# Performance work log

Hardware: AMD Instinct MI355X
Metric: run time of the kernel (lower is better)

## Reference

```python
import jax, jax.numpy as jnp
import numpy as np

N = 100000   # nodes
E = 1600000  # edges (avg degree 16)
DIN = 128
DH = 64


def setup_inputs() -> dict:
    key = jax.random.key(0)
    ks = jax.random.split(key, 6)
    x = jax.random.normal(ks[0], (N, DIN), dtype=jnp.float32)
    edge_index = jax.random.randint(ks[1], (2, E), 0, N, dtype=jnp.int32)
    W1 = jax.random.normal(ks[2], (DIN, DH), dtype=jnp.float32) * (1.0 / np.sqrt(DIN))
    b1 = jnp.zeros((DH,), dtype=jnp.float32)
    W2 = jax.random.normal(ks[3], (DH, DH), dtype=jnp.float32) * (1.0 / np.sqrt(DH))
    b2 = jnp.zeros((DH,), dtype=jnp.float32)
    alpha = jnp.full((DH,), 0.25, dtype=jnp.float32)  # PReLU per-channel slope (torch default 0.25)
    return {"x": x, "edge_index": edge_index, "W1": W1, "b1": b1, "W2": W2, "b2": b2, "alpha": alpha}


def _gcn_layer(h, src, dst, norm, W, b):
    # GCNConv: linear transform, then normalized scatter-add aggregation, then bias
    h = h @ W                                  # [N, dout]
    msg = h[src] * norm[:, None]               # [E+N, dout] gathered + scaled messages
    agg = jax.ops.segment_sum(msg, dst, num_segments=N)
    return agg + b


def reference(x, edge_index, W1, b1, W2, b2, alpha):
    src0, dst0 = edge_index[0], edge_index[1]
    # GCNConv default: add self-loops, symmetric normalization deg^{-1/2} A deg^{-1/2}
    loops = jnp.arange(N, dtype=src0.dtype)
    src = jnp.concatenate([src0, loops])
    dst = jnp.concatenate([dst0, loops])
    ones = jnp.ones(src.shape[0], dtype=x.dtype)
    deg = jax.ops.segment_sum(ones, dst, num_segments=N)
    dinv = jnp.where(deg > 0, jax.lax.rsqrt(deg), 0.0)
    norm = dinv[src] * dinv[dst]               # [E+N]

    prelu = lambda z: jnp.where(z >= 0, z, alpha * z)  # shared per-channel PReLU
    z = prelu(_gcn_layer(x, src, dst, norm, W1, b1))
    z = prelu(_gcn_layer(z, src, dst, norm, W2, b2))
    return z
```

## Files before the change

kernel.cpp:

```cpp
#include <hip/hip_runtime.h>
#include <hip/hip_bf16.h>

#define NN 100000
#define NE 1600000
#define NBUCK 391
#define CAP 5056
#define CHUNK 2048
#define PBLOCKS 782
#define MMBLOCKS 782
#define BCUR_STRIDE 16

typedef __attribute__((ext_vector_type(8))) short short8;
typedef __attribute__((ext_vector_type(4))) float f32x4;

static __device__ __forceinline__ unsigned short f2bf(float f) {
    unsigned u = __float_as_uint(f);
    unsigned r = (u + 0x7fffu + ((u >> 16) & 1u)) >> 16;
    return (unsigned short)r;
}
static __device__ __forceinline__ float bf_lo(unsigned u) {
    return __uint_as_float(u << 16);
}
static __device__ __forceinline__ float bf_hi(unsigned u) {
    return __uint_as_float(u & 0xffff0000u);
}
static __device__ __forceinline__ void acc8(float* acc, uint4 v, float nm) {
    acc[0] += bf_lo(v.x) * nm; acc[1] += bf_hi(v.x) * nm;
    acc[2] += bf_lo(v.y) * nm; acc[3] += bf_hi(v.y) * nm;
    acc[4] += bf_lo(v.z) * nm; acc[5] += bf_hi(v.z) * nm;
    acc[6] += bf_lo(v.w) * nm; acc[7] += bf_hi(v.w) * nm;
}
static __device__ __forceinline__ void acc8a(float* acc, uint4 v) {
    acc[0] += bf_lo(v.x); acc[1] += bf_hi(v.x);
    acc[2] += bf_lo(v.y); acc[3] += bf_hi(v.y);
    acc[4] += bf_lo(v.z); acc[5] += bf_hi(v.z);
    acc[6] += bf_lo(v.w); acc[7] += bf_hi(v.w);
}

template<bool SCALED>
static __device__ __forceinline__ void agg_loop(const unsigned char* hb,
                                                const int* __restrict__ esrc,
                                                const float* __restrict__ dinv,
                                                int start, int cnt, float dn,
                                                float* acc) {
    int i = 0;
    for (; i + 4 <= cnt; i += 4) {
        int s0 = esrc[start + i];
        int s1 = esrc[start + i + 1];
        int s2 = esrc[start + i + 2];
        int s3 = esrc[start + i + 3];
        uint4 w0 = *(const uint4*)(hb + ((unsigned)s0 << 7));
        uint4 w1 = *(const uint4*)(hb + ((unsigned)s1 << 7));
        uint4 w2 = *(const uint4*)(hb + ((unsigned)s2 << 7));
        uint4 w3 = *(const uint4*)(hb + ((unsigned)s3 << 7));
        if constexpr (SCALED) {
            acc8a(acc, w0); acc8a(acc, w1); acc8a(acc, w2); acc8a(acc, w3);
        } else {
            float n0 = dinv[s0] * dn, n1 = dinv[s1] * dn;
            float n2 = dinv[s2] * dn, n3 = dinv[s3] * dn;
            acc8(acc, w0, n0); acc8(acc, w1, n1); acc8(acc, w2, n2); acc8(acc, w3, n3);
        }
    }
    for (; i < cnt; ++i) {
        int s0 = esrc[start + i];
        uint4 w0 = *(const uint4*)(hb + ((unsigned)s0 << 7));
        if constexpr (SCALED) {
            acc8a(acc, w0);
        } else {
            float n0 = dinv[s0] * dn;
            acc8(acc, w0, n0);
        }
    }
}

__global__ __launch_bounds__(256) void k_fat(const int* __restrict__ ei,
                                             int* __restrict__ bcur,
                                             unsigned* __restrict__ ebuf,
                                             const float* __restrict__ x,
                                             const float* __restrict__ W1,
                                             unsigned short* __restrict__ hout) {
    __shared__ __attribute__((aligned(16))) unsigned char smem[19584];
    int tid = threadIdx.x;
    if (blockIdx.x < PBLOCKS) {
        int* lexc  = (int*)smem;
        int* lbase = (int*)(smem + 1564);
        unsigned* sv = (unsigned*)(smem + 3128);
        int* sd    = (int*)(smem + 11320);
        int* wscan = (int*)(smem + 19512);
        int* sTot  = (int*)(smem + 19528);

        int e0 = blockIdx.x * CHUNK;
        for (int i = tid; i < NBUCK; i += 256) lexc[i] = 0;
        __syncthreads();
        int bs[8]; int rs[8]; unsigned ps[8];
        #pragma unroll
        for (int k = 0; k < 8; ++k) {
            int e = e0 + k * 256 + tid;
            bs[k] = -1;
            if (e < NE) {
                int d = ei[NE + e];
                int s = ei[e];
                int b = d >> 8;
                bs[k] = b;
                rs[k] = atomicAdd(&lexc[b], 1);
                ps[k] = ((unsigned)s << 8) | (unsigned)(d & 255);
            }
        }
        __syncthreads();
        int b0i = 2 * tid, b1i = 2 * tid + 1;
        int c0 = (b0i < NBUCK) ? lexc[b0i] : 0;
        int c1 = (b1i < NBUCK) ? lexc[b1i] : 0;
        int v = c0 + c1;
        int lane = tid & 63;
        int incl = v;
        #pragma unroll
        for (int off = 1; off < 64; off <<= 1) {
            int t = __shfl_up(incl, off, 64);
            if (lane >= off) incl += t;
        }
        if (lane == 63) wscan[tid >> 6] = incl;
        int gb0 = 0, gb1 = 0;
        if (c0) gb0 = atomicAdd(&bcur[b0i * BCUR_STRIDE], c0);
        if (c1) gb1 = atomicAdd(&bcur[b1i * BCUR_STRIDE], c1);
        __syncthreads();
        if (tid == 0) {
            int a = 0;
            #pragma unroll
            for (int w = 0; w < 4; ++w) { int t = wscan[w]; wscan[w] = a; a += t; }
            *sTot = a;
        }
        __syncthreads();
        int ex = incl - v + wscan[tid >> 6];
        if (b0i < NBUCK) { lexc[b0i] = ex;      lbase[b0i] = gb0; }
        if (b1i < NBUCK) { lexc[b1i] = ex + c0; lbase[b1i] = gb1; }
        __syncthreads();
        #pragma unroll
        for (int k = 0; k < 8; ++k) {
            if (bs[k] >= 0) {
                int b = bs[k];
                int slot = lexc[b] + rs[k];
                int pos  = lbase[b] + rs[k];
                sv[slot] = ps[k];
                sd[slot] = (pos < CAP) ? b * CAP + pos : -1;
            }
        }
        __syncthreads();
        int V = *sTot;
        for (int j = tid; j < V; j += 256) {
            int d = sd[j];
            if (d >= 0) ebuf[d] = sv[j];
        }
    } else {
        constexpr int K = 128, KP = K + 8;
        unsigned short* Wt = (unsigned short*)smem;
        for (int idx = tid; idx < K * 64; idx += 256) {
            int k = idx >> 6, n = idx & 63;
            Wt[n * KP + k] = f2bf(W1[idx]);
        }
        __syncthreads();
        int wave = tid >> 6, lane = tid & 63;
        int m = lane & 15, q = lane >> 4;
        int nb = (blockIdx.x - PBLOCKS) * 128 + wave * 32;
        #pragma unroll
        for (int rt = 0; rt < 2; ++rt) {
            int n0 = nb + rt * 16;
            f32x4 acc[4] = {{0.f,0.f,0.f,0.f},{0.f,0.f,0.f,0.f},{0.f,0.f,0.f,0.f},{0.f,0.f,0.f,0.f}};
            int row = n0 + m;
            int rowc = row < NN ? row : NN - 1;
            const float* xr = x + (long)rowc * K;
            #pragma unroll
            for (int kk = 0; kk < K / 32; ++kk) {
                const float4* p = (const float4*)(xr + kk * 32 + q * 8);
                float4 v0 = p[0], v1 = p[1];
                float xv[8] = {v0.x, v0.y, v0.z, v0.w, v1.x, v1.y, v1.z, v1.w};
                short8 afrag;
                #pragma unroll
                for (int i2 = 0; i2 < 8; ++i2) afrag[i2] = (short)f2bf(xv[i2]);
                #pragma unroll
                for (int nt = 0; nt < 4; ++nt) {
                    const short8* bp = (const short8*)&Wt[(nt * 16 + m) * KP + kk * 32 + q * 8];
                    acc[nt] = __builtin_amdgcn_mfma_f32_16x16x32_bf16(afrag, *bp, acc[nt], 0, 0, 0);
                }
            }
            #pragma unroll
            for (int reg = 0; reg < 4; ++reg) {
                int node = n0 + q * 4 + reg;
                if (node < NN) {
                    #pragma unroll
                    for (int nt = 0; nt < 4; ++nt)
                        hout[(long)node * 64 + nt * 16 + m] = f2bf(acc[nt][reg]);
                }
            }
        }
    }
}

__global__ __launch_bounds__(256) void k_build(const int* __restrict__ bcur,
                                               const unsigned* __restrict__ ebuf,
                                               unsigned* __restrict__ rowinfo,
                                               float* __restrict__ dinv,
                                               int* __restrict__ esrc) {
    __shared__ int cnt[2048];
    __shared__ int kstart[2048];
    __shared__ int wsum[4];
    int tid = threadIdx.x;
    int base = blockIdx.x * CAP;
    int nedge = bcur[blockIdx.x * BCUR_STRIDE];
    if (nedge > CAP) nedge = CAP;
    #pragma unroll
    for (int t = 0; t < 8; ++t) cnt[(tid << 3) | t] = 0;
    __syncthreads();
    int st[20];
    int ssrc[20];
    #pragma unroll
    for (int k = 0; k < 20; ++k) {
        int j = tid + k * 256;
        st[k] = -1;
        if (j < nedge) {
            unsigned p = ebuf[base + j];
            int dl = (int)(p & 255u);
            int s = (int)(p >> 8);
            int key = (dl << 3) | (s >> 14);
            int r = atomicAdd(&cnt[key], 1);
            st[k] = (r << 11) | key;
            ssrc[k] = s;
        }
    }
    __syncthreads();
    int c[8];
    int v = 0;
    #pragma unroll
    for (int t = 0; t < 8; ++t) { c[t] = cnt[(tid << 3) | t]; v += c[t]; }
    int lane = tid & 63;
    int incl = v;
    #pragma unroll
    for (int off = 1; off < 64; off <<= 1) {
        int t = __shfl_up(incl, off, 64);
        if (lane >= off) incl += t;
    }
    if (lane == 63) wsum[tid >> 6] = incl;
    __syncthreads();
    if (tid == 0) {
        int a = 0;
        #pragma unroll
        for (int w = 0; w < 4; ++w) { int t = wsum[w]; wsum[w] = a; a += t; }
    }
    __syncthreads();
    int ex = incl - v + wsum[tid >> 6];
    int node = blockIdx.x * 256 + tid;
    if (node < NN) {
        rowinfo[node] = ((unsigned)(base + ex) << 11) | (unsigned)v;
        dinv[node] = rsqrtf((float)(v + 1));
    }
    int off = base + ex;
    #pragma unroll
    for (int t = 0; t < 8; ++t) { kstart[(tid << 3) | t] = off; off += c[t]; }
    __syncthreads();
    #pragma unroll
    for (int k = 0; k < 20; ++k) {
        if (st[k] >= 0)
            esrc[kstart[st[k] & 2047] + (st[k] >> 11)] = ssrc[k];
    }
}

__global__ __launch_bounds__(256) void k_aggmm(const unsigned* __restrict__ rowinfo,
                                               const int* __restrict__ esrc,
                                               const unsigned short* __restrict__ h,
                                               const float* __restrict__ dinv,
                                               const float* __restrict__ bias,
                                               const float* __restrict__ alpha,
                                               const float* __restrict__ W2,
                                               unsigned short* __restrict__ hout2) {
    __shared__ unsigned short Wt[64 * 72];
    __shared__ unsigned short aggs[32 * 72];
    __shared__ float dnv[32];
    int tid = threadIdx.x;
    for (int idx = tid; idx < 64 * 64; idx += 256) {
        int k = idx >> 6, n = idx & 63;
        Wt[n * 72 + k] = f2bf(W2[idx]);
    }
    int sl = tid & 7;
    int ln = tid >> 3;
    int node = blockIdx.x * 32 + ln;
    unsigned u = rowinfo[node];
    int start = (int)(u >> 11);
    int cnt = (int)(u & 2047u);
    float dn = dinv[node];
    if (sl == 0) dnv[ln] = dn;
    const unsigned char* hb = (const unsigned char*)h + sl * 16;

    float acc[8];
    {
        uint4 hw = *(const uint4*)(hb + ((unsigned)node << 7));
        float d2 = dn * dn;
        acc[0] = bf_lo(hw.x) * d2; acc[1] = bf_hi(hw.x) * d2;
        acc[2] = bf_lo(hw.y) * d2; acc[3] = bf_hi(hw.y) * d2;
        acc[4] = bf_lo(hw.z) * d2; acc[5] = bf_hi(hw.z) * d2;
        acc[6] = bf_lo(hw.w) * d2; acc[7] = bf_hi(hw.w) * d2;
    }
    agg_loop<false>(hb, esrc, dinv, start, cnt, dn, acc);

    float4 blo = *(const float4*)(bias + sl * 8);
    float4 bhi = *(const float4*)(bias + sl * 8 + 4);
    float4 alo = *(const float4*)(alpha + sl * 8);
    float4 ahi = *(const float4*)(alpha + sl * 8 + 4);
    float bb[8] = {blo.x, blo.y, blo.z, blo.w, bhi.x, bhi.y, bhi.z, bhi.w};
    float aa[8] = {alo.x, alo.y, alo.z, alo.w, ahi.x, ahi.y, ahi.z, ahi.w};
    #pragma unroll
    for (int j = 0; j < 8; ++j) {
        float v = acc[j] + bb[j];
        acc[j] = v >= 0.f ? v : aa[j] * v;
    }
    uint4 pk;
    pk.x = (unsigned)f2bf(acc[0]) | ((unsigned)f2bf(acc[1]) << 16);
    pk.y = (unsigned)f2bf(acc[2]) | ((unsigned)f2bf(acc[3]) << 16);
    pk.z = (unsigned)f2bf(acc[4]) | ((unsigned)f2bf(acc[5]) << 16);
    pk.w = (unsigned)f2bf(acc[6]) | ((unsigned)f2bf(acc[7]) << 16);
    *(uint4*)&aggs[ln * 72 + sl * 8] = pk;
    __syncthreads();

    int wave = tid >> 6;
    if (wave < 2) {
        int lane = tid & 63;
        int m = lane & 15, q = lane >> 4;
        int row = wave * 16 + m;
        f32x4 c2[4] = {{0.f,0.f,0.f,0.f},{0.f,0.f,0.f,0.f},{0.f,0.f,0.f,0.f},{0.f,0.f,0.f,0.f}};
        #pragma unroll
        for (int kk = 0; kk < 2; ++kk) {
            short8 afrag = *(const short8*)&aggs[row * 72 + kk * 32 + q * 8];
            #pragma unroll
            for (int nt = 0; nt < 4; ++nt) {
                const short8* bp = (const short8*)&Wt[(nt * 16 + m) * 72 + kk * 32 + q * 8];
                c2[nt] = __builtin_amdgcn_mfma_f32_16x16x32_bf16(afrag, *bp, c2[nt], 0, 0, 0);
            }
        }
        #pragma unroll
        for (int reg = 0; reg < 4; ++reg) {
            int nd = blockIdx.x * 32 + wave * 16 + q * 4 + reg;
            float dv = dnv[wave * 16 + q * 4 + reg];
            #pragma unroll
            for (int nt = 0; nt < 4; ++nt)
                hout2[(long)nd * 64 + nt * 16 + m] = f2bf(c2[nt][reg] * dv);
        }
    }
}

__global__ __launch_bounds__(256) void k_agg2(const unsigned* __restrict__ rowinfo,
                                              const int* __restrict__ esrc,
                                              const unsigned short* __restrict__ h,
                                              const float* __restrict__ dinv,
                                              const float* __restrict__ bias,
                                              const float* __restrict__ alpha,
                                              float* __restrict__ out) {
    int sl = threadIdx.x & 7;
    int node = blockIdx.x * 32 + (threadIdx.x >> 3);
    unsigned u = rowinfo[node];
    int start = (int)(u >> 11);
    int cnt = (int)(u & 2047u);
    float dn = dinv[node];
    const unsigned char* hb = (const unsigned char*)h + sl * 16;

    float acc[8];
    {
        uint4 hw = *(const uint4*)(hb + ((unsigned)node << 7));
        acc[0] = bf_lo(hw.x); acc[1] = bf_hi(hw.x);
        acc[2] = bf_lo(hw.y); acc[3] = bf_hi(hw.y);
        acc[4] = bf_lo(hw.z); acc[5] = bf_hi(hw.z);
        acc[6] = bf_lo(hw.w); acc[7] = bf_hi(hw.w);
    }
    agg_loop<true>(hb, esrc, dinv, start, cnt, dn, acc);

    float4 blo = *(const float4*)(bias + sl * 8);
    float4 bhi = *(const float4*)(bias + sl * 8 + 4);
    float4 alo = *(const float4*)(alpha + sl * 8);
    float4 ahi = *(const float4*)(alpha + sl * 8 + 4);
    float bb[8] = {blo.x, blo.y, blo.z, blo.w, bhi.x, bhi.y, bhi.z, bhi.w};
    float aa[8] = {alo.x, alo.y, alo.z, alo.w, ahi.x, ahi.y, ahi.z, ahi.w};
    #pragma unroll
    for (int j = 0; j < 8; ++j) {
        float v = acc[j] * dn + bb[j];
        acc[j] = v >= 0.f ? v : aa[j] * v;
    }
    float* op = out + (long)node * 64 + sl * 8;
    *(float4*)op = make_float4(acc[0], acc[1], acc[2], acc[3]);
    *(float4*)(op + 4) = make_float4(acc[4], acc[5], acc[6], acc[7]);
}

extern "C" void kernel_launch(void* const* d_in, const int* in_sizes, int n_in,
                              void* d_out, int out_size, void* d_ws, size_t ws_size,
                              hipStream_t stream) {
    const float* x     = (const float*)d_in[0];
    const int*   ei    = (const int*)d_in[1];
    const float* W1    = (const float*)d_in[2];
    const float* b1    = (const float*)d_in[3];
    const float* W2    = (const float*)d_in[4];
    const float* b2    = (const float*)d_in[5];
    const float* alpha = (const float*)d_in[6];
    float* out = (float*)d_out;

    char* ws = (char*)d_ws;
    float*    dinv      = (float*)(ws);
    unsigned* rowinfo   = (unsigned*)(ws + 400384);
    int*      bcur      = (int*)(ws + 800768);
    int*      esrc      = (int*)(ws + 825856);
    unsigned short* hbf = (unsigned short*)(ws + 8733440);
    unsigned* ebuf      = (unsigned*)(ws + 21533440);
    unsigned short* hbf2 = (unsigned short*)(ws + 21533440);

    (void)hipMemsetAsync(bcur, 0, NBUCK * BCUR_STRIDE * sizeof(int), stream);
    k_fat<<<PBLOCKS + MMBLOCKS, 256, 0, stream>>>(ei, bcur, ebuf, x, W1, hbf);
    k_build<<<NBUCK, 256, 0, stream>>>(bcur, ebuf, rowinfo, dinv, esrc);
    k_aggmm<<<NN / 32, 256, 0, stream>>>(rowinfo, esrc, hbf, dinv, b1, alpha, W2, hbf2);
    k_agg2<<<NN / 32, 256, 0, stream>>>(rowinfo, esrc, hbf2, dinv, b2, alpha, out);
}
```

Baseline: 218.6 us.

## Sort nodes by degree for aggregation load balance and shrink matmul tiles

Adds a degree histogram in k_build and a new k_perm kernel that builds a permutation of nodes grouped by in-degree. Both aggregation kernels then process nodes in that order, so the nodes sharing a block or wave have similar edge counts and fewer lanes sit idle. Separately, the first-layer matmul blocks now cover 64 rows instead of 128, doubling the block count. The cost is one extra launch, scattered output writes and a loss of locality in the node order.

```diff
diff --git a/kernel.cpp b/kernel.cpp
--- a/kernel.cpp
+++ b/kernel.cpp
@@ -7,7 +7,7 @@
 #define CAP 5056
 #define CHUNK 2048
 #define PBLOCKS 782
-#define MMBLOCKS 782
+#define MMBLOCKS 1563
 #define BCUR_STRIDE 16
 
 typedef __attribute__((ext_vector_type(8))) short short8;
@@ -160,36 +160,32 @@
         __syncthreads();
         int wave = tid >> 6, lane = tid & 63;
         int m = lane & 15, q = lane >> 4;
-        int nb = (blockIdx.x - PBLOCKS) * 128 + wave * 32;
-        #pragma unroll
-        for (int rt = 0; rt < 2; ++rt) {
-            int n0 = nb + rt * 16;
-            f32x4 acc[4] = {{0.f,0.f,0.f,0.f},{0.f,0.f,0.f,0.f},{0.f,0.f,0.f,0.f},{0.f,0.f,0.f,0.f}};
-            int row = n0 + m;
-            int rowc = row < NN ? row : NN - 1;
-            const float* xr = x + (long)rowc * K;
+        int n0 = (blockIdx.x - PBLOCKS) * 64 + wave * 16;
+        f32x4 acc[4] = {{0.f,0.f,0.f,0.f},{0.f,0.f,0.f,0.f},{0.f,0.f,0.f,0.f},{0.f,0.f,0.f,0.f}};
+        int row = n0 + m;
+        int rowc = row < NN ? row : NN - 1;
+        const float* xr = x + (long)rowc * K;
+        #pragma unroll
+        for (int kk = 0; kk < K / 32; ++kk) {
+            const float4* p = (const float4*)(xr + kk * 32 + q * 8);
+            float4 v0 = p[0], v1 = p[1];
+            float xv[8] = {v0.x, v0.y, v0.z, v0.w, v1.x, v1.y, v1.z, v1.w};
+            short8 afrag;
             #pragma unroll
-            for (int kk = 0; kk < K / 32; ++kk) {
-                const float4* p = (const float4*)(xr + kk * 32 + q * 8);
-                float4 v0 = p[0], v1 = p[1];
-                float xv[8] = {v0.x, v0.y, v0.z, v0.w, v1.x, v1.y, v1.z, v1.w};
-                short8 afrag;
+            for (int i2 = 0; i2 < 8; ++i2) afrag[i2] = (short)f2bf(xv[i2]);
+            #pragma unroll
+            for (int nt = 0; nt < 4; ++nt) {
+                const short8* bp = (const short8*)&Wt[(nt * 16 + m) * KP + kk * 32 + q * 8];
+                acc[nt] = __builtin_amdgcn_mfma_f32_16x16x32_bf16(afrag, *bp, acc[nt], 0, 0, 0);
+            }
+        }
+        #pragma unroll
+        for (int reg = 0; reg < 4; ++reg) {
+            int node = n0 + q * 4 + reg;
+            if (node < NN) {
                 #pragma unroll
-                for (int i2 = 0; i2 < 8; ++i2) afrag[i2] = (short)f2bf(xv[i2]);
-                #pragma unroll
-                for (int nt = 0; nt < 4; ++nt) {
-                    const short8* bp = (const short8*)&Wt[(nt * 16 + m) * KP + kk * 32 + q * 8];
-                    acc[nt] = __builtin_amdgcn_mfma_f32_16x16x32_bf16(afrag, *bp, acc[nt], 0, 0, 0);
-                }
-            }
-            #pragma unroll
-            for (int reg = 0; reg < 4; ++reg) {
-                int node = n0 + q * 4 + reg;
-                if (node < NN) {
-                    #pragma unroll
-                    for (int nt = 0; nt < 4; ++nt)
-                        hout[(long)node * 64 + nt * 16 + m] = f2bf(acc[nt][reg]);
-                }
+                for (int nt = 0; nt < 4; ++nt)
+                    hout[(long)node * 64 + nt * 16 + m] = f2bf(acc[nt][reg]);
             }
         }
     }
@@ -199,16 +195,19 @@
                                                const unsigned* __restrict__ ebuf,
                                                unsigned* __restrict__ rowinfo,
                                                float* __restrict__ dinv,
-                                               int* __restrict__ esrc) {
+                                               int* __restrict__ esrc,
+                                               int* __restrict__ dhist) {
     __shared__ int cnt[2048];
     __shared__ int kstart[2048];
     __shared__ int wsum[4];
+    __shared__ int lhist[256];
     int tid = threadIdx.x;
     int base = blockIdx.x * CAP;
     int nedge = bcur[blockIdx.x * BCUR_STRIDE];
     if (nedge > CAP) nedge = CAP;
     #pragma unroll
     for (int t = 0; t < 8; ++t) cnt[(tid << 3) | t] = 0;
+    lhist[tid] = 0;
     __syncthreads();
     int st[20];
     int ssrc[20];
@@ -251,6 +250,7 @@
     if (node < NN) {
         rowinfo[node] = ((unsigned)(base + ex) << 11) | (unsigned)v;
         dinv[node] = rsqrtf((float)(v + 1));
+        atomicAdd(&lhist[v < 255 ? v : 255], 1);
     }
     int off = base + ex;
     #pragma unroll
@@ -261,6 +261,50 @@
         if (st[k] >= 0)
             esrc[kstart[st[k] & 2047] + (st[k] >> 11)] = ssrc[k];
     }
+    int hc = lhist[tid];
+    if (hc) atomicAdd(&dhist[tid * 16], hc);
+}
+
+__global__ __launch_bounds__(256) void k_perm(const unsigned* __restrict__ rowinfo,
+                                              const int* __restrict__ dhist,
+                                              int* __restrict__ binpos,
+                                              int* __restrict__ perm) {
+    __shared__ int lh[256];
+    __shared__ int gb[256];
+    __shared__ int wsum[4];
+    int tid = threadIdx.x;
+    lh[tid] = 0;
+    __syncthreads();
+    int node = blockIdx.x * 256 + tid;
+    int bin = 0, rank = 0;
+    bool live = node < NN;
+    if (live) {
+        int deg = (int)(rowinfo[node] & 2047u);
+        bin = deg < 255 ? deg : 255;
+        rank = atomicAdd(&lh[bin], 1);
+    }
+    __syncthreads();
+    int c = lh[tid];
+    int h = dhist[tid * 16];
+    int lane = tid & 63;
+    int incl = h;
+    #pragma unroll
+    for (int off = 1; off < 64; off <<= 1) {
+        int t = __shfl_up(incl, off, 64);
+        if (lane >= off) incl += t;
+    }
+    if (lane == 63) wsum[tid >> 6] = incl;
+    __syncthreads();
+    if (tid == 0) {
+        int a = 0;
+        #pragma unroll
+        for (int w = 0; w < 4; ++w) { int t = wsum[w]; wsum[w] = a; a += t; }
+    }
+    __syncthreads();
+    int dbase = incl - h + wsum[tid >> 6];
+    gb[tid] = dbase + (c ? atomicAdd(&binpos[tid * 16], c) : 0);
+    __syncthreads();
+    if (live) perm[gb[bin] + rank] = node;
 }
 
 __global__ __launch_bounds__(256) void k_aggmm(const unsigned* __restrict__ rowinfo,
@@ -270,10 +314,12 @@
                                                const float* __restrict__ bias,
                                                const float* __restrict__ alpha,
                                                const float* __restrict__ W2,
+                                               const int* __restrict__ perm,
                                                unsigned short* __restrict__ hout2) {
     __shared__ unsigned short Wt[64 * 72];
     __shared__ unsigned short aggs[32 * 72];
     __shared__ float dnv[32];
+    __shared__ int pnode[32];
     int tid = threadIdx.x;
     for (int idx = tid; idx < 64 * 64; idx += 256) {
         int k = idx >> 6, n = idx & 63;
@@ -281,12 +327,12 @@
     }
     int sl = tid & 7;
     int ln = tid >> 3;
-    int node = blockIdx.x * 32 + ln;
+    int node = perm[blockIdx.x * 32 + ln];
     unsigned u = rowinfo[node];
     int start = (int)(u >> 11);
     int cnt = (int)(u & 2047u);
     float dn = dinv[node];
-    if (sl == 0) dnv[ln] = dn;
+    if (sl == 0) { dnv[ln] = dn; pnode[ln] = node; }
     const unsigned char* hb = (const unsigned char*)h + sl * 16;
 
     float acc[8];
@@ -336,8 +382,9 @@
         }
         #pragma unroll
         for (int reg = 0; reg < 4; ++reg) {
-            int nd = blockIdx.x * 32 + wave * 16 + q * 4 + reg;
-            float dv = dnv[wave * 16 + q * 4 + reg];
+            int rr = wave * 16 + q * 4 + reg;
+            int nd = pnode[rr];
+            float dv = dnv[rr];
             #pragma unroll
             for (int nt = 0; nt < 4; ++nt)
                 hout2[(long)nd * 64 + nt * 16 + m] = f2bf(c2[nt][reg] * dv);
@@ -351,9 +398,10 @@
                                               const float* __restrict__ dinv,
                                               const float* __restrict__ bias,
                                               const float* __restrict__ alpha,
+                                              const int* __restrict__ perm,
                                               float* __restrict__ out) {
     int sl = threadIdx.x & 7;
-    int node = blockIdx.x * 32 + (threadIdx.x >> 3);
+    int node = perm[blockIdx.x * 32 + (threadIdx.x >> 3)];
     unsigned u = rowinfo[node];
     int start = (int)(u >> 11);
     int cnt = (int)(u & 2047u);
@@ -402,14 +450,18 @@
     float*    dinv      = (float*)(ws);
     unsigned* rowinfo   = (unsigned*)(ws + 400384);
     int*      bcur      = (int*)(ws + 800768);
-    int*      esrc      = (int*)(ws + 825856);
-    unsigned short* hbf = (unsigned short*)(ws + 8733440);
-    unsigned* ebuf      = (unsigned*)(ws + 21533440);
-    unsigned short* hbf2 = (unsigned short*)(ws + 21533440);
-
-    (void)hipMemsetAsync(bcur, 0, NBUCK * BCUR_STRIDE * sizeof(int), stream);
+    int*      dhist     = (int*)(ws + 825856);
+    int*      binpos    = (int*)(ws + 842240);
+    int*      perm      = (int*)(ws + 858624);
+    int*      esrc      = (int*)(ws + 1259008);
+    unsigned short* hbf = (unsigned short*)(ws + 9166592);
+    unsigned* ebuf      = (unsigned*)(ws + 21966592);
+    unsigned short* hbf2 = (unsigned short*)(ws + 21966592);
+
+    (void)hipMemsetAsync(bcur, 0, 25088 + 16384 + 16384, stream);
     k_fat<<<PBLOCKS + MMBLOCKS, 256, 0, stream>>>(ei, bcur, ebuf, x, W1, hbf);
-    k_build<<<NBUCK, 256, 0, stream>>>(bcur, ebuf, rowinfo, dinv, esrc);
-    k_aggmm<<<NN / 32, 256, 0, stream>>>(rowinfo, esrc, hbf, dinv, b1, alpha, W2, hbf2);
-    k_agg2<<<NN / 32, 256, 0, stream>>>(rowinfo, esrc, hbf2, dinv, b2, alpha, out);
-}
+    k_build<<<NBUCK, 256, 0, stream>>>(bcur, ebuf, rowinfo, dinv, esrc, dhist);
+    k_perm<<<NBUCK, 256, 0, stream>>>(rowinfo, dhist, binpos, perm);
+    k_aggmm<<<NN / 32, 256, 0, stream>>>(rowinfo, esrc, hbf, dinv, b1, alpha, W2, perm, hbf2);
+    k_agg2<<<NN / 32, 256, 0, stream>>>(rowinfo, esrc, hbf2, dinv, b2, alpha, perm, out);
+}
```

New measurement: 229.9 us. 1.05x slower.
